# Performance work log

Hardware: AMD Instinct MI355X
Metric: run time of the kernel (lower is better)

The kernel has to match this reference:

```python
import jax, jax.numpy as jnp
import numpy as np

GROUPS = 32
EPS = 1e-5


def group_norm(x, scale, bias):
    # x: [B, C, T]
    b, c, t = x.shape
    xg = x.reshape(b, GROUPS, c // GROUPS, t)
    mean = xg.mean(axis=(2, 3), keepdims=True)
    var = xg.var(axis=(2, 3), keepdims=True)
    xg = (xg - mean) * jax.lax.rsqrt(var + EPS)
    return xg.reshape(b, c, t) * scale[None, :, None] + bias[None, :, None]


def setup_inputs() -> dict:
    key = jax.random.key(0)
    ks = jax.random.split(key, 7)
    B, C, H, W = 8, 512, 32, 32
    x = jax.random.normal(ks[0], (B, C, H, W), dtype=jnp.float32)
    gn_scale = jnp.ones((C,), jnp.float32)
    gn_bias = jnp.zeros((C,), jnp.float32)
    qkv_w = jax.random.normal(ks[1], (3 * C, C), jnp.float32) / np.sqrt(C)
    qkv_b = jnp.zeros((3 * C,), jnp.float32)
    # proj_out is zero-initialized in the original; use small random weights
    # so the attention path contributes to the output (trained-model behavior).
    proj_w = jax.random.normal(ks[2], (C, C), jnp.float32) / np.sqrt(C)
    proj_b = jnp.zeros((C,), jnp.float32)
    return {"x": x, "gn_scale": gn_scale, "gn_bias": gn_bias,
            "qkv_w": qkv_w, "qkv_b": qkv_b, "proj_w": proj_w, "proj_b": proj_b}


def reference(x, gn_scale, gn_bias, qkv_w, qkv_b, proj_w, proj_b):
    NUM_HEADS = 8
    b, c, *spatial = x.shape
    t = int(np.prod(spatial))
    xf = x.reshape(b, c, t)                                   # [B,C,T]
    xn = group_norm(xf, gn_scale, gn_bias)
    qkv = jnp.einsum('oc,bct->bot', qkv_w, xn) + qkv_b[None, :, None]  # [B,3C,T]
    # legacy layout: reshape to heads BEFORE splitting into q,k,v thirds
    qkv = qkv.reshape(b * NUM_HEADS, -1, t)                   # [B*H, 3C/H, T]
    ch = qkv.shape[1] // 3
    q, k, v = jnp.split(qkv, 3, axis=1)                       # each [B*H, ch, T]
    scale = 1.0 / np.sqrt(np.sqrt(ch))
    w = jnp.einsum('bct,bcs->bts', q * scale, k * scale)      # [B*H, T, T]
    w = jax.nn.softmax(w.astype(jnp.float32), axis=-1).astype(w.dtype)
    h = jnp.einsum('bts,bcs->bct', w, v)                      # [B*H, ch, T]
    h = h.reshape(b, c, t)
    h = jnp.einsum('oc,bct->bot', proj_w, h) + proj_b[None, :, None]
    return (xf + h).reshape(b, c, *spatial)
```

## Files before the change

kernel.cpp:

```cpp
#include <hip/hip_runtime.h>

typedef __bf16 bf16;
typedef __attribute__((ext_vector_type(8))) __bf16 bf16x8;
typedef __attribute__((ext_vector_type(4))) __bf16 bf16x4;
typedef __attribute__((ext_vector_type(4))) float f32x4;

#define MFMA(a, b, c) __builtin_amdgcn_mfma_f32_16x16x32_bf16(a, b, c, 0, 0, 0)
#define GLOAD_LDS(g, l)                                                        \
  __builtin_amdgcn_global_load_lds(                                            \
      (const __attribute__((address_space(1))) void*)(g),                      \
      (__attribute__((address_space(3))) void*)(l), 16, 0, 0)

#if __has_builtin(__builtin_amdgcn_exp2f)
#define EXP2(x) __builtin_amdgcn_exp2f(x)
#else
#define EXP2(x) exp2f(x)
#endif

#define C1LOG 0.18033688011f

__device__ __forceinline__ int swz64(int row, int col) {
  return row * 64 + (col ^ ((row & 7) << 3));
}

__global__ __launch_bounds__(256, 2) void k_pre(
    const float* __restrict__ x, const float* __restrict__ gs,
    const float* __restrict__ gb, const float* __restrict__ qw,
    const float* __restrict__ pw, bf16* __restrict__ xnT,
    bf16* __restrict__ wq, bf16* __restrict__ wp) {
  int tid = threadIdx.x;
  if (blockIdx.x >= 256) {
    int i = (blockIdx.x - 256) * 256 + tid;
    int idx = i * 4;
    float4 v;
    bf16* o;
    if (idx < 786432) {
      v = *(const float4*)(qw + idx);
      o = wq + idx;
    } else {
      int j = idx - 786432;
      v = *(const float4*)(pw + j);
      o = wp + j;
    }
    o[0] = (bf16)v.x; o[1] = (bf16)v.y; o[2] = (bf16)v.z; o[3] = (bf16)v.w;
    return;
  }
  __shared__ float xs[16 * 1024];
  __shared__ float red[2][4];
  int blk = blockIdx.x;
  int b = blk >> 5, g = blk & 31;
  const float* xp = x + ((size_t)(b * 512 + g * 16)) * 1024;
  float s = 0.f, ss = 0.f;
  for (int i = tid; i < 4096; i += 256) {
    float4 v = ((const float4*)xp)[i];
    *(float4*)&xs[i * 4] = v;
    s += v.x + v.y + v.z + v.w;
    ss += v.x * v.x + v.y * v.y + v.z * v.z + v.w * v.w;
  }
#pragma unroll
  for (int m = 1; m < 64; m <<= 1) {
    s += __shfl_xor(s, m);
    ss += __shfl_xor(ss, m);
  }
  int wid = tid >> 6;
  if ((tid & 63) == 0) { red[0][wid] = s; red[1][wid] = ss; }
  __syncthreads();
  float fs = red[0][0] + red[0][1] + red[0][2] + red[0][3];
  float fss = red[1][0] + red[1][1] + red[1][2] + red[1][3];
  float mean = fs * (1.f / 16384.f);
  float var = fss * (1.f / 16384.f) - mean * mean;
  float inv = rsqrtf(var + 1e-5f);
  float a_[16], b_[16];
#pragma unroll
  for (int cl = 0; cl < 16; ++cl) {
    float sc = gs[g * 16 + cl] * inv;
    a_[cl] = sc;
    b_[cl] = gb[g * 16 + cl] - mean * sc;
  }
  int t0 = tid * 4;
  bf16 tmp[4][16];
#pragma unroll
  for (int cl = 0; cl < 16; ++cl) {
    float4 v = *(float4*)&xs[cl * 1024 + t0];
    tmp[0][cl] = (bf16)(v.x * a_[cl] + b_[cl]);
    tmp[1][cl] = (bf16)(v.y * a_[cl] + b_[cl]);
    tmp[2][cl] = (bf16)(v.z * a_[cl] + b_[cl]);
    tmp[3][cl] = (bf16)(v.w * a_[cl] + b_[cl]);
  }
  bf16* outp = xnT + (size_t)b * 1024 * 512 + g * 16;
#pragma unroll
  for (int k = 0; k < 4; ++k) {
    *(bf16x8*)(outp + (size_t)(t0 + k) * 512) = *(bf16x8*)&tmp[k][0];
    *(bf16x8*)(outp + (size_t)(t0 + k) * 512 + 8) = *(bf16x8*)&tmp[k][8];
  }
}

__global__ void k_qkv(const bf16* __restrict__ xnT, const bf16* __restrict__ wq,
                      const float* __restrict__ qb, bf16* __restrict__ qkvT,
                      bf16* __restrict__ vTout) {
  int bid = blockIdx.x;
  int swz = (bid & 7) * 96 + (bid >> 3);
  int nt = swz % 12, mt = swz / 12;
  int tid = threadIdx.x, lane = tid & 63;
  int wid = tid >> 6, wr = wid >> 1, wc = wid & 1;
  int lr = lane & 15, lk8 = (lane >> 4) * 8, prow4 = (lane >> 4) * 4;
  __shared__ __align__(16) bf16 lA[8192], lB[8192];
  const bf16* Ab = xnT + (size_t)mt * 128 * 512;
  const bf16* Bb = wq + (size_t)nt * 128 * 512;
  f32x4 acc[4][4] = {};
  int ubase = tid & 192;
  for (int kt = 0; kt < 8; ++kt) {
    __syncthreads();
#pragma unroll
    for (int i = 0; i < 4; ++i) {
      int s = i * 256 + tid;
      int r = s >> 3, cc = (s & 7) ^ (r & 7);
      GLOAD_LDS(Ab + (size_t)r * 512 + kt * 64 + cc * 8, lA + (i * 256 + ubase) * 8);
      GLOAD_LDS(Bb + (size_t)r * 512 + kt * 64 + cc * 8, lB + (i * 256 + ubase) * 8);
    }
    __syncthreads();
#pragma unroll
    for (int ksl = 0; ksl < 2; ++ksl) {
      bf16x8 aF[4], bF[4];
#pragma unroll
      for (int m = 0; m < 4; ++m)
        aF[m] = *(bf16x8*)&lA[swz64(wr * 64 + m * 16 + lr, ksl * 32 + lk8)];
#pragma unroll
      for (int n = 0; n < 4; ++n)
        bF[n] = *(bf16x8*)&lB[swz64(wc * 64 + n * 16 + lr, ksl * 32 + lk8)];
      __builtin_amdgcn_s_setprio(1);
#pragma unroll
      for (int m = 0; m < 4; ++m)
#pragma unroll
        for (int n = 0; n < 4; ++n) acc[m][n] = MFMA(aF[m], bF[n], acc[m][n]);
      __builtin_amdgcn_s_setprio(0);
    }
  }
#pragma unroll
  for (int n = 0; n < 4; ++n) {
    int o = nt * 128 + wc * 64 + n * 16 + lr;
    float bias = qb[o];
    int hh = o / 192;
    int om = o - hh * 192;
    bool isv = om >= 128;
    float scl = (om >= 64 && om < 128) ? C1LOG : 1.0f;
    int c = om - 128;
#pragma unroll
    for (int m = 0; m < 4; ++m) {
      int row0 = mt * 128 + wr * 64 + m * 16 + prow4;
      if (isv) {
        int bb = row0 >> 10, t0 = row0 & 1023;
        bf16x4 v4;
#pragma unroll
        for (int r = 0; r < 4; ++r) v4[r] = (bf16)(acc[m][n][r] + bias);
        *(bf16x4*)&vTout[(((size_t)bb * 8 + hh) * 64 + c) * 1024 + t0] = v4;
      } else {
#pragma unroll
        for (int r = 0; r < 4; ++r)
          qkvT[(size_t)(row0 + r) * 1536 + o] = (bf16)((acc[m][n][r] + bias) * scl);
      }
    }
  }
}

__global__ __launch_bounds__(512, 4) void k_attn(const bf16* __restrict__ qkvT,
                                                 const bf16* __restrict__ vT,
                                                 bf16* __restrict__ hT) {
  int d = blockIdx.x;
  int head = (d & 7) * 8 + (d >> 6);
  int qt = (d >> 3) & 7;
  int b = head >> 3, hh = head & 7;
  int tid = threadIdx.x, lane = tid & 63, wid = tid >> 6;
  int lr = lane & 15, hi = lane >> 4, lk8 = hi * 8;

  __shared__ __align__(16) bf16 KT[2][8192];
  __shared__ __align__(16) bf16 VTl[2][8192];
  __shared__ __align__(16) bf16 PT[8][1024];

  const bf16* qbase = qkvT + (size_t)b * 1024 * 1536 + hh * 192;
  const bf16* kbase = qbase + 64;
  const bf16* vbase = vT + (size_t)head * 64 * 1024;

  int tq = qt * 128 + wid * 16 + lr;
  bf16x8 qf0 = *(const bf16x8*)(qbase + (size_t)tq * 1536 + lk8);
  bf16x8 qf1 = *(const bf16x8*)(qbase + (size_t)tq * 1536 + 32 + lk8);

  f32x4 hacc[4] = {};
  f32x4 lsum = {};
  float m2 = -1e30f;

  int rr8 = tid >> 3;
  int cc_ = (tid & 7) ^ (rr8 & 7);
  const bf16* ksrcT = kbase + (size_t)rr8 * 1536 + cc_ * 8;
  const bf16* vsrcT = vbase + (size_t)rr8 * 1024 + cc_ * 8;
  int ldst = wid * 512;

  bf16x8 ones;
#pragma unroll
  for (int j = 0; j < 8; ++j) ones[j] = (bf16)1.0f;

  GLOAD_LDS(ksrcT, KT[0] + ldst);
  GLOAD_LDS(ksrcT + (size_t)64 * 1536, KT[0] + 4096 + ldst);
  GLOAD_LDS(vsrcT, VTl[0] + ldst);
  GLOAD_LDS(vsrcT + 64, VTl[0] + 4096 + ldst);

  for (int it = 0; it < 8; ++it) {
    int cur = it & 1;
    asm volatile("s_waitcnt vmcnt(0)" ::: "memory");
    __builtin_amdgcn_s_barrier();
    __builtin_amdgcn_sched_barrier(0);
    if (it < 7) {
      size_t sb = (size_t)(it + 1) * 128;
      const bf16* kp = ksrcT + sb * 1536;
      const bf16* vp = vsrcT + sb;
      GLOAD_LDS(kp, KT[cur ^ 1] + ldst);
      GLOAD_LDS(kp + (size_t)64 * 1536, KT[cur ^ 1] + 4096 + ldst);
      GLOAD_LDS(vp, VTl[cur ^ 1] + ldst);
      GLOAD_LDS(vp + 64, VTl[cur ^ 1] + 4096 + ldst);
    }
    f32x4 sc[8];
#pragma unroll
    for (int n = 0; n < 8; ++n) sc[n] = f32x4{0.f, 0.f, 0.f, 0.f};
    __builtin_amdgcn_s_setprio(1);
#pragma unroll
    for (int n = 0; n < 8; ++n) {
      bf16x8 kA0 = *(bf16x8*)&KT[cur][swz64(n * 16 + lr, lk8)];
      bf16x8 kA1 = *(bf16x8*)&KT[cur][swz64(n * 16 + lr, 32 + lk8)];
      sc[n] = MFMA(kA0, qf0, sc[n]);
      sc[n] = MFMA(kA1, qf1, sc[n]);
    }
    __builtin_amdgcn_s_setprio(0);
    float a0 = fmaxf(fmaxf(sc[0][0], sc[0][1]), fmaxf(sc[0][2], sc[0][3]));
    float a1 = fmaxf(fmaxf(sc[1][0], sc[1][1]), fmaxf(sc[1][2], sc[1][3]));
    float a2 = fmaxf(fmaxf(sc[2][0], sc[2][1]), fmaxf(sc[2][2], sc[2][3]));
    float a3 = fmaxf(fmaxf(sc[3][0], sc[3][1]), fmaxf(sc[3][2], sc[3][3]));
    float a4 = fmaxf(fmaxf(sc[4][0], sc[4][1]), fmaxf(sc[4][2], sc[4][3]));
    float a5 = fmaxf(fmaxf(sc[5][0], sc[5][1]), fmaxf(sc[5][2], sc[5][3]));
    float a6 = fmaxf(fmaxf(sc[6][0], sc[6][1]), fmaxf(sc[6][2], sc[6][3]));
    float a7 = fmaxf(fmaxf(sc[7][0], sc[7][1]), fmaxf(sc[7][2], sc[7][3]));
    float tm = fmaxf(fmaxf(fmaxf(a0, a1), fmaxf(a2, a3)),
                     fmaxf(fmaxf(a4, a5), fmaxf(a6, a7)));
    tm = fmaxf(tm, __shfl_xor(tm, 16));
    tm = fmaxf(tm, __shfl_xor(tm, 32));
    if (__any(tm > m2 + 7.213f)) {
      float mn = fmaxf(m2, tm);
      float al = EXP2(m2 - mn);
      m2 = mn;
      lsum[0] *= al; lsum[1] *= al; lsum[2] *= al; lsum[3] *= al;
#pragma unroll
      for (int n = 0; n < 4; ++n) {
        hacc[n][0] *= al; hacc[n][1] *= al; hacc[n][2] *= al; hacc[n][3] *= al;
      }
    }
#pragma unroll
    for (int h = 0; h < 2; ++h) {
#pragma unroll
      for (int n4 = 0; n4 < 4; ++n4) {
        int n = 4 * h + n4;
        bf16x4 p4;
        p4[0] = (bf16)EXP2(sc[n][0] - m2);
        p4[1] = (bf16)EXP2(sc[n][1] - m2);
        p4[2] = (bf16)EXP2(sc[n][2] - m2);
        p4[3] = (bf16)EXP2(sc[n][3] - m2);
        *(bf16x4*)&PT[wid][swz64(lr, n4 * 16 + hi * 4)] = p4;
      }
      asm volatile("s_waitcnt lgkmcnt(0)" ::: "memory");
      __builtin_amdgcn_sched_barrier(0);
      bf16x8 pa0 = *(bf16x8*)&PT[wid][swz64(lr, lk8)];
      bf16x8 pa1 = *(bf16x8*)&PT[wid][swz64(lr, 32 + lk8)];
      const bf16* vb = VTl[cur] + h * 4096;
      __builtin_amdgcn_s_setprio(1);
#pragma unroll
      for (int n4 = 0; n4 < 4; ++n4) {
        bf16x8 vA0 = *(bf16x8*)&vb[swz64(n4 * 16 + lr, lk8)];
        bf16x8 vA1 = *(bf16x8*)&vb[swz64(n4 * 16 + lr, 32 + lk8)];
        hacc[n4] = MFMA(vA0, pa0, hacc[n4]);
        hacc[n4] = MFMA(vA1, pa1, hacc[n4]);
      }
      lsum = MFMA(ones, pa0, lsum);
      lsum = MFMA(ones, pa1, lsum);
      __builtin_amdgcn_s_setprio(0);
    }
  }
  float invl = 1.f / lsum[0];
  bf16* dst = hT + ((size_t)b * 1024 + tq) * 512 + hh * 64 + hi * 4;
#pragma unroll
  for (int n = 0; n < 4; ++n) {
    bf16x4 o4;
#pragma unroll
    for (int r = 0; r < 4; ++r) o4[r] = (bf16)(hacc[n][r] * invl);
    *(bf16x4*)(dst + n * 16) = o4;
  }
}

__global__ void k_proj(const bf16* __restrict__ hT, const bf16* __restrict__ wp,
                       const float* __restrict__ pb, const float* __restrict__ x,
                       float* __restrict__ out) {
  int bid = blockIdx.x;
  int swz = (bid & 7) * 64 + (bid >> 3);
  int nt = swz & 7, mt = swz >> 3;
  int tid = threadIdx.x, lane = tid & 63;
  int wid = tid >> 6, wr = wid >> 1, wc = wid & 1;
  int lr = lane & 15, lk8 = (lane >> 4) * 8, prow4 = (lane >> 4) * 4;
  __shared__ __align__(16) bf16 lA[8192], lB[4096];
  const bf16* Ab = hT + (size_t)mt * 128 * 512;
  const bf16* Bb = wp + (size_t)nt * 64 * 512;
  f32x4 acc[4][2] = {};
  int ubase = tid & 192;
  for (int kt = 0; kt < 8; ++kt) {
    __syncthreads();
#pragma unroll
    for (int i = 0; i < 4; ++i) {
      int s = i * 256 + tid;
      int r = s >> 3, cc = (s & 7) ^ (r & 7);
      GLOAD_LDS(Ab + (size_t)r * 512 + kt * 64 + cc * 8, lA + (i * 256 + ubase) * 8);
    }
#pragma unroll
    for (int i = 0; i < 2; ++i) {
      int s = i * 256 + tid;
      int r = s >> 3, cc = (s & 7) ^ (r & 7);
      GLOAD_LDS(Bb + (size_t)r * 512 + kt * 64 + cc * 8, lB + (i * 256 + ubase) * 8);
    }
    __syncthreads();
#pragma unroll
    for (int ksl = 0; ksl < 2; ++ksl) {
      bf16x8 aF[4], bF[2];
#pragma unroll
      for (int m = 0; m < 4; ++m)
        aF[m] = *(bf16x8*)&lA[swz64(wr * 64 + m * 16 + lr, ksl * 32 + lk8)];
#pragma unroll
      for (int n = 0; n < 2; ++n)
        bF[n] = *(bf16x8*)&lB[swz64(wc * 32 + n * 16 + lr, ksl * 32 + lk8)];
      __builtin_amdgcn_s_setprio(1);
#pragma unroll
      for (int m = 0; m < 4; ++m)
#pragma unroll
        for (int n = 0; n < 2; ++n) acc[m][n] = MFMA(aF[m], bF[n], acc[m][n]);
      __builtin_amdgcn_s_setprio(0);
    }
  }
#pragma unroll
  for (int n = 0; n < 2; ++n) {
    int o = nt * 64 + wc * 32 + n * 16 + lr;
    float bias = pb[o];
#pragma unroll
    for (int m = 0; m < 4; ++m) {
      int row0 = mt * 128 + wr * 64 + m * 16 + prow4;
      int bb = row0 >> 10, t0 = row0 & 1023;
      size_t off = ((size_t)bb * 512 + o) * 1024 + t0;
      float4 xv = *(const float4*)(x + off);
      float4 rr;
      rr.x = acc[m][n][0] + xv.x + bias;
      rr.y = acc[m][n][1] + xv.y + bias;
      rr.z = acc[m][n][2] + xv.z + bias;
      rr.w = acc[m][n][3] + xv.w + bias;
      *(float4*)(out + off) = rr;
    }
  }
}

extern "C" void kernel_launch(void* const* d_in, const int* in_sizes, int n_in,
                              void* d_out, int out_size, void* d_ws, size_t ws_size,
                              hipStream_t stream) {
  const float* x = (const float*)d_in[0];
  const float* gs = (const float*)d_in[1];
  const float* gb = (const float*)d_in[2];
  const float* qw = (const float*)d_in[3];
  const float* qb = (const float*)d_in[4];
  const float* pw = (const float*)d_in[5];
  const float* pb = (const float*)d_in[6];
  float* out = (float*)d_out;
  char* ws = (char*)d_ws;
  bf16* xnT  = (bf16*)(ws);
  bf16* qkvT = (bf16*)(ws + 8388608);
  bf16* vT   = (bf16*)(ws + 33554432);
  bf16* hT   = (bf16*)(ws + 41943040);
  bf16* wq   = (bf16*)(ws + 50331648);
  bf16* wp   = (bf16*)(ws + 51904512);

  k_pre<<<1280, 256, 0, stream>>>(x, gs, gb, qw, pw, xnT, wq, wp);
  k_qkv<<<768, 256, 0, stream>>>(xnT, wq, qb, qkvT, vT);
  k_attn<<<512, 512, 0, stream>>>(qkvT, vT, hT);
  k_proj<<<512, 256, 0, stream>>>(hT, wp, pb, x, out);
}
```

Measured before the change: 74.09 us.

## Process two query sub-tiles per wave in attention to reuse K/V fragments

The attention kernel now runs 4 waves of 256 threads per block instead of 8 waves. Each wave handles 32 query rows as two 16-row groups, so every K and V fragment read from LDS feeds twice as many MFMAs. The global-to-LDS loads are split across more iterations per thread to match the smaller block. This raises register pressure, from two sets of score and accumulator tiles, and halves the number of waves per block available to hide latency.

```diff
diff --git a/kernel.cpp b/kernel.cpp
--- a/kernel.cpp
+++ b/kernel.cpp
@@ -163,7 +163,7 @@
   }
 }
 
-__global__ __launch_bounds__(512, 4) void k_attn(const bf16* __restrict__ qkvT,
+__global__ __launch_bounds__(256, 2) void k_attn(const bf16* __restrict__ qkvT,
                                                  const bf16* __restrict__ vT,
                                                  bf16* __restrict__ hT) {
   int d = blockIdx.x;
@@ -181,28 +181,37 @@
   const bf16* kbase = qbase + 64;
   const bf16* vbase = vT + (size_t)head * 64 * 1024;
 
-  int tq = qt * 128 + wid * 16 + lr;
-  bf16x8 qf0 = *(const bf16x8*)(qbase + (size_t)tq * 1536 + lk8);
-  bf16x8 qf1 = *(const bf16x8*)(qbase + (size_t)tq * 1536 + 32 + lk8);
-
-  f32x4 hacc[4] = {};
-  f32x4 lsum = {};
-  float m2 = -1e30f;
+  int tq0 = qt * 128 + wid * 32 + lr;
+  int tq1 = tq0 + 16;
+  bf16x8 qf[2][2];
+  qf[0][0] = *(const bf16x8*)(qbase + (size_t)tq0 * 1536 + lk8);
+  qf[0][1] = *(const bf16x8*)(qbase + (size_t)tq0 * 1536 + 32 + lk8);
+  qf[1][0] = *(const bf16x8*)(qbase + (size_t)tq1 * 1536 + lk8);
+  qf[1][1] = *(const bf16x8*)(qbase + (size_t)tq1 * 1536 + 32 + lk8);
+
+  f32x4 hacc[2][4] = {};
+  f32x4 lsum[2] = {};
+  float m2[2] = {-1e30f, -1e30f};
 
   int rr8 = tid >> 3;
   int cc_ = (tid & 7) ^ (rr8 & 7);
-  const bf16* ksrcT = kbase + (size_t)rr8 * 1536 + cc_ * 8;
-  const bf16* vsrcT = vbase + (size_t)rr8 * 1024 + cc_ * 8;
+  const bf16* ks = kbase + (size_t)rr8 * 1536 + cc_ * 8;
+  const bf16* vs0 = vbase + (size_t)rr8 * 1024 + cc_ * 8;
+  const bf16* vs1 = vs0 + 64;
   int ldst = wid * 512;
 
   bf16x8 ones;
 #pragma unroll
   for (int j = 0; j < 8; ++j) ones[j] = (bf16)1.0f;
 
-  GLOAD_LDS(ksrcT, KT[0] + ldst);
-  GLOAD_LDS(ksrcT + (size_t)64 * 1536, KT[0] + 4096 + ldst);
-  GLOAD_LDS(vsrcT, VTl[0] + ldst);
-  GLOAD_LDS(vsrcT + 64, VTl[0] + 4096 + ldst);
+#pragma unroll
+  for (int i = 0; i < 4; ++i)
+    GLOAD_LDS(ks + (size_t)i * 32 * 1536, KT[0] + i * 2048 + ldst);
+#pragma unroll
+  for (int i = 0; i < 2; ++i) {
+    GLOAD_LDS(vs0 + (size_t)i * 32 * 1024, VTl[0] + i * 2048 + ldst);
+    GLOAD_LDS(vs1 + (size_t)i * 32 * 1024, VTl[0] + 4096 + i * 2048 + ldst);
+  }
 
   for (int it = 0; it < 8; ++it) {
     int cur = it & 1;
@@ -211,45 +220,60 @@
     __builtin_amdgcn_sched_barrier(0);
     if (it < 7) {
       size_t sb = (size_t)(it + 1) * 128;
-      const bf16* kp = ksrcT + sb * 1536;
-      const bf16* vp = vsrcT + sb;
-      GLOAD_LDS(kp, KT[cur ^ 1] + ldst);
-      GLOAD_LDS(kp + (size_t)64 * 1536, KT[cur ^ 1] + 4096 + ldst);
-      GLOAD_LDS(vp, VTl[cur ^ 1] + ldst);
-      GLOAD_LDS(vp + 64, VTl[cur ^ 1] + 4096 + ldst);
-    }
-    f32x4 sc[8];
-#pragma unroll
-    for (int n = 0; n < 8; ++n) sc[n] = f32x4{0.f, 0.f, 0.f, 0.f};
+      const bf16* kp = ks + sb * 1536;
+#pragma unroll
+      for (int i = 0; i < 4; ++i)
+        GLOAD_LDS(kp + (size_t)i * 32 * 1536, KT[cur ^ 1] + i * 2048 + ldst);
+#pragma unroll
+      for (int i = 0; i < 2; ++i) {
+        GLOAD_LDS(vs0 + sb + (size_t)i * 32 * 1024,
+                  VTl[cur ^ 1] + i * 2048 + ldst);
+        GLOAD_LDS(vs1 + sb + (size_t)i * 32 * 1024,
+                  VTl[cur ^ 1] + 4096 + i * 2048 + ldst);
+      }
+    }
+    f32x4 s0[8], s1[8];
+#pragma unroll
+    for (int n = 0; n < 8; ++n) {
+      s0[n] = f32x4{0.f, 0.f, 0.f, 0.f};
+      s1[n] = f32x4{0.f, 0.f, 0.f, 0.f};
+    }
     __builtin_amdgcn_s_setprio(1);
 #pragma unroll
     for (int n = 0; n < 8; ++n) {
       bf16x8 kA0 = *(bf16x8*)&KT[cur][swz64(n * 16 + lr, lk8)];
       bf16x8 kA1 = *(bf16x8*)&KT[cur][swz64(n * 16 + lr, 32 + lk8)];
-      sc[n] = MFMA(kA0, qf0, sc[n]);
-      sc[n] = MFMA(kA1, qf1, sc[n]);
+      s0[n] = MFMA(kA0, qf[0][0], s0[n]);
+      s0[n] = MFMA(kA1, qf[0][1], s0[n]);
+      s1[n] = MFMA(kA0, qf[1][0], s1[n]);
+      s1[n] = MFMA(kA1, qf[1][1], s1[n]);
     }
     __builtin_amdgcn_s_setprio(0);
-    float a0 = fmaxf(fmaxf(sc[0][0], sc[0][1]), fmaxf(sc[0][2], sc[0][3]));
-    float a1 = fmaxf(fmaxf(sc[1][0], sc[1][1]), fmaxf(sc[1][2], sc[1][3]));
-    float a2 = fmaxf(fmaxf(sc[2][0], sc[2][1]), fmaxf(sc[2][2], sc[2][3]));
-    float a3 = fmaxf(fmaxf(sc[3][0], sc[3][1]), fmaxf(sc[3][2], sc[3][3]));
-    float a4 = fmaxf(fmaxf(sc[4][0], sc[4][1]), fmaxf(sc[4][2], sc[4][3]));
-    float a5 = fmaxf(fmaxf(sc[5][0], sc[5][1]), fmaxf(sc[5][2], sc[5][3]));
-    float a6 = fmaxf(fmaxf(sc[6][0], sc[6][1]), fmaxf(sc[6][2], sc[6][3]));
-    float a7 = fmaxf(fmaxf(sc[7][0], sc[7][1]), fmaxf(sc[7][2], sc[7][3]));
-    float tm = fmaxf(fmaxf(fmaxf(a0, a1), fmaxf(a2, a3)),
-                     fmaxf(fmaxf(a4, a5), fmaxf(a6, a7)));
-    tm = fmaxf(tm, __shfl_xor(tm, 16));
-    tm = fmaxf(tm, __shfl_xor(tm, 32));
-    if (__any(tm > m2 + 7.213f)) {
-      float mn = fmaxf(m2, tm);
-      float al = EXP2(m2 - mn);
-      m2 = mn;
-      lsum[0] *= al; lsum[1] *= al; lsum[2] *= al; lsum[3] *= al;
-#pragma unroll
-      for (int n = 0; n < 4; ++n) {
-        hacc[n][0] *= al; hacc[n][1] *= al; hacc[n][2] *= al; hacc[n][3] *= al;
+#pragma unroll
+    for (int g = 0; g < 2; ++g) {
+      f32x4* sg = g ? s1 : s0;
+      float a0 = fmaxf(fmaxf(sg[0][0], sg[0][1]), fmaxf(sg[0][2], sg[0][3]));
+      float a1 = fmaxf(fmaxf(sg[1][0], sg[1][1]), fmaxf(sg[1][2], sg[1][3]));
+      float a2 = fmaxf(fmaxf(sg[2][0], sg[2][1]), fmaxf(sg[2][2], sg[2][3]));
+      float a3 = fmaxf(fmaxf(sg[3][0], sg[3][1]), fmaxf(sg[3][2], sg[3][3]));
+      float a4 = fmaxf(fmaxf(sg[4][0], sg[4][1]), fmaxf(sg[4][2], sg[4][3]));
+      float a5 = fmaxf(fmaxf(sg[5][0], sg[5][1]), fmaxf(sg[5][2], sg[5][3]));
+      float a6 = fmaxf(fmaxf(sg[6][0], sg[6][1]), fmaxf(sg[6][2], sg[6][3]));
+      float a7 = fmaxf(fmaxf(sg[7][0], sg[7][1]), fmaxf(sg[7][2], sg[7][3]));
+      float tm = fmaxf(fmaxf(fmaxf(a0, a1), fmaxf(a2, a3)),
+                       fmaxf(fmaxf(a4, a5), fmaxf(a6, a7)));
+      tm = fmaxf(tm, __shfl_xor(tm, 16));
+      tm = fmaxf(tm, __shfl_xor(tm, 32));
+      if (__any(tm > m2[g] + 7.213f)) {
+        float mn = fmaxf(m2[g], tm);
+        float al = EXP2(m2[g] - mn);
+        m2[g] = mn;
+        lsum[g][0] *= al; lsum[g][1] *= al; lsum[g][2] *= al; lsum[g][3] *= al;
+#pragma unroll
+        for (int n = 0; n < 4; ++n) {
+          hacc[g][n][0] *= al; hacc[g][n][1] *= al;
+          hacc[g][n][2] *= al; hacc[g][n][3] *= al;
+        }
       }
     }
 #pragma unroll
@@ -258,38 +282,54 @@
       for (int n4 = 0; n4 < 4; ++n4) {
         int n = 4 * h + n4;
         bf16x4 p4;
-        p4[0] = (bf16)EXP2(sc[n][0] - m2);
-        p4[1] = (bf16)EXP2(sc[n][1] - m2);
-        p4[2] = (bf16)EXP2(sc[n][2] - m2);
-        p4[3] = (bf16)EXP2(sc[n][3] - m2);
-        *(bf16x4*)&PT[wid][swz64(lr, n4 * 16 + hi * 4)] = p4;
+        p4[0] = (bf16)EXP2(s0[n][0] - m2[0]);
+        p4[1] = (bf16)EXP2(s0[n][1] - m2[0]);
+        p4[2] = (bf16)EXP2(s0[n][2] - m2[0]);
+        p4[3] = (bf16)EXP2(s0[n][3] - m2[0]);
+        *(bf16x4*)&PT[wid * 2][swz64(lr, n4 * 16 + hi * 4)] = p4;
+        bf16x4 q4;
+        q4[0] = (bf16)EXP2(s1[n][0] - m2[1]);
+        q4[1] = (bf16)EXP2(s1[n][1] - m2[1]);
+        q4[2] = (bf16)EXP2(s1[n][2] - m2[1]);
+        q4[3] = (bf16)EXP2(s1[n][3] - m2[1]);
+        *(bf16x4*)&PT[wid * 2 + 1][swz64(lr, n4 * 16 + hi * 4)] = q4;
       }
       asm volatile("s_waitcnt lgkmcnt(0)" ::: "memory");
       __builtin_amdgcn_sched_barrier(0);
-      bf16x8 pa0 = *(bf16x8*)&PT[wid][swz64(lr, lk8)];
-      bf16x8 pa1 = *(bf16x8*)&PT[wid][swz64(lr, 32 + lk8)];
+      bf16x8 pa00 = *(bf16x8*)&PT[wid * 2][swz64(lr, lk8)];
+      bf16x8 pa01 = *(bf16x8*)&PT[wid * 2][swz64(lr, 32 + lk8)];
+      bf16x8 pa10 = *(bf16x8*)&PT[wid * 2 + 1][swz64(lr, lk8)];
+      bf16x8 pa11 = *(bf16x8*)&PT[wid * 2 + 1][swz64(lr, 32 + lk8)];
       const bf16* vb = VTl[cur] + h * 4096;
       __builtin_amdgcn_s_setprio(1);
 #pragma unroll
       for (int n4 = 0; n4 < 4; ++n4) {
         bf16x8 vA0 = *(bf16x8*)&vb[swz64(n4 * 16 + lr, lk8)];
         bf16x8 vA1 = *(bf16x8*)&vb[swz64(n4 * 16 + lr, 32 + lk8)];
-        hacc[n4] = MFMA(vA0, pa0, hacc[n4]);
-        hacc[n4] = MFMA(vA1, pa1, hacc[n4]);
+        hacc[0][n4] = MFMA(vA0, pa00, hacc[0][n4]);
+        hacc[0][n4] = MFMA(vA1, pa01, hacc[0][n4]);
+        hacc[1][n4] = MFMA(vA0, pa10, hacc[1][n4]);
+        hacc[1][n4] = MFMA(vA1, pa11, hacc[1][n4]);
       }
-      lsum = MFMA(ones, pa0, lsum);
-      lsum = MFMA(ones, pa1, lsum);
+      lsum[0] = MFMA(ones, pa00, lsum[0]);
+      lsum[0] = MFMA(ones, pa01, lsum[0]);
+      lsum[1] = MFMA(ones, pa10, lsum[1]);
+      lsum[1] = MFMA(ones, pa11, lsum[1]);
       __builtin_amdgcn_s_setprio(0);
     }
   }
-  float invl = 1.f / lsum[0];
-  bf16* dst = hT + ((size_t)b * 1024 + tq) * 512 + hh * 64 + hi * 4;
-#pragma unroll
-  for (int n = 0; n < 4; ++n) {
-    bf16x4 o4;
-#pragma unroll
-    for (int r = 0; r < 4; ++r) o4[r] = (bf16)(hacc[n][r] * invl);
-    *(bf16x4*)(dst + n * 16) = o4;
+#pragma unroll
+  for (int g = 0; g < 2; ++g) {
+    float invl = 1.f / lsum[g][0];
+    int tq = g ? tq1 : tq0;
+    bf16* dst = hT + ((size_t)b * 1024 + tq) * 512 + hh * 64 + hi * 4;
+#pragma unroll
+    for (int n = 0; n < 4; ++n) {
+      bf16x4 o4;
+#pragma unroll
+      for (int r = 0; r < 4; ++r) o4[r] = (bf16)(hacc[g][n][r] * invl);
+      *(bf16x4*)(dst + n * 16) = o4;
+    }
   }
 }
 
@@ -380,6 +420,6 @@
 
   k_pre<<<1280, 256, 0, stream>>>(x, gs, gb, qw, pw, xnT, wq, wp);
   k_qkv<<<768, 256, 0, stream>>>(xnT, wq, qb, qkvT, vT);
-  k_attn<<<512, 512, 0, stream>>>(qkvT, vT, hT);
+  k_attn<<<512, 256, 0, stream>>>(qkvT, vT, hT);
   k_proj<<<512, 256, 0, stream>>>(hT, wp, pb, x, out);
 }
```

Measured after the change: 75.76 us. 2.3% more time.

## Retile QKV GEMM to 256-row blocks and shrink attention blocks to 64 queries

Applied to the files above, without the earlier changes.

The QKV GEMM now uses 512-thread blocks covering 256 rows by 128 columns, which halves the grid and reuses each weight tile across twice as many rows. The attention kernel switches to 256-thread blocks handling 64 queries each, streaming K/V in 64-key chunks over 16 iterations. This doubles the attention grid to 1024 blocks and halves its LDS footprint, aiming for more resident blocks and better load balance across CUs. The cost is more barrier and loop overhead per key processed in attention, and a larger LDS tile in the GEMM.

```diff
diff --git a/kernel.cpp b/kernel.cpp
--- a/kernel.cpp
+++ b/kernel.cpp
@@ -99,24 +99,30 @@
                       const float* __restrict__ qb, bf16* __restrict__ qkvT,
                       bf16* __restrict__ vTout) {
   int bid = blockIdx.x;
-  int swz = (bid & 7) * 96 + (bid >> 3);
+  int swz = (bid & 7) * 48 + (bid >> 3);
   int nt = swz % 12, mt = swz / 12;
   int tid = threadIdx.x, lane = tid & 63;
   int wid = tid >> 6, wr = wid >> 1, wc = wid & 1;
   int lr = lane & 15, lk8 = (lane >> 4) * 8, prow4 = (lane >> 4) * 4;
-  __shared__ __align__(16) bf16 lA[8192], lB[8192];
-  const bf16* Ab = xnT + (size_t)mt * 128 * 512;
+  __shared__ __align__(16) bf16 lA[16384], lB[8192];
+  const bf16* Ab = xnT + (size_t)mt * 256 * 512;
   const bf16* Bb = wq + (size_t)nt * 128 * 512;
   f32x4 acc[4][4] = {};
-  int ubase = tid & 192;
+  int ubase = tid & 448;
+  int r8 = tid >> 3, c8 = tid & 7;
   for (int kt = 0; kt < 8; ++kt) {
     __syncthreads();
 #pragma unroll
     for (int i = 0; i < 4; ++i) {
-      int s = i * 256 + tid;
-      int r = s >> 3, cc = (s & 7) ^ (r & 7);
-      GLOAD_LDS(Ab + (size_t)r * 512 + kt * 64 + cc * 8, lA + (i * 256 + ubase) * 8);
-      GLOAD_LDS(Bb + (size_t)r * 512 + kt * 64 + cc * 8, lB + (i * 256 + ubase) * 8);
+      int r = i * 64 + r8, cc = c8 ^ (r8 & 7);
+      GLOAD_LDS(Ab + (size_t)r * 512 + kt * 64 + cc * 8,
+                lA + (i * 512 + ubase) * 8);
+    }
+#pragma unroll
+    for (int i = 0; i < 2; ++i) {
+      int r = i * 64 + r8, cc = c8 ^ (r8 & 7);
+      GLOAD_LDS(Bb + (size_t)r * 512 + kt * 64 + cc * 8,
+                lB + (i * 512 + ubase) * 8);
     }
     __syncthreads();
 #pragma unroll
@@ -147,7 +153,7 @@
     int c = om - 128;
 #pragma unroll
     for (int m = 0; m < 4; ++m) {
-      int row0 = mt * 128 + wr * 64 + m * 16 + prow4;
+      int row0 = mt * 256 + wr * 64 + m * 16 + prow4;
       if (isv) {
         int bb = row0 >> 10, t0 = row0 & 1023;
         bf16x4 v4;
@@ -163,25 +169,26 @@
   }
 }
 
-__global__ __launch_bounds__(512, 4) void k_attn(const bf16* __restrict__ qkvT,
+__global__ __launch_bounds__(256, 4) void k_attn(const bf16* __restrict__ qkvT,
                                                  const bf16* __restrict__ vT,
                                                  bf16* __restrict__ hT) {
   int d = blockIdx.x;
-  int head = (d & 7) * 8 + (d >> 6);
-  int qt = (d >> 3) & 7;
+  int within = d >> 3;
+  int head = (d & 7) * 8 + (within >> 4);
+  int qt = within & 15;
   int b = head >> 3, hh = head & 7;
   int tid = threadIdx.x, lane = tid & 63, wid = tid >> 6;
   int lr = lane & 15, hi = lane >> 4, lk8 = hi * 8;
 
-  __shared__ __align__(16) bf16 KT[2][8192];
-  __shared__ __align__(16) bf16 VTl[2][8192];
-  __shared__ __align__(16) bf16 PT[8][1024];
+  __shared__ __align__(16) bf16 KT[2][4096];
+  __shared__ __align__(16) bf16 VTl[2][4096];
+  __shared__ __align__(16) bf16 PT[4][1024];
 
   const bf16* qbase = qkvT + (size_t)b * 1024 * 1536 + hh * 192;
   const bf16* kbase = qbase + 64;
   const bf16* vbase = vT + (size_t)head * 64 * 1024;
 
-  int tq = qt * 128 + wid * 16 + lr;
+  int tq = qt * 64 + wid * 16 + lr;
   bf16x8 qf0 = *(const bf16x8*)(qbase + (size_t)tq * 1536 + lk8);
   bf16x8 qf1 = *(const bf16x8*)(qbase + (size_t)tq * 1536 + 32 + lk8);
 
@@ -191,39 +198,40 @@
 
   int rr8 = tid >> 3;
   int cc_ = (tid & 7) ^ (rr8 & 7);
-  const bf16* ksrcT = kbase + (size_t)rr8 * 1536 + cc_ * 8;
-  const bf16* vsrcT = vbase + (size_t)rr8 * 1024 + cc_ * 8;
+  const bf16* ks = kbase + (size_t)rr8 * 1536 + cc_ * 8;
+  const bf16* vs = vbase + (size_t)rr8 * 1024 + cc_ * 8;
   int ldst = wid * 512;
 
   bf16x8 ones;
 #pragma unroll
   for (int j = 0; j < 8; ++j) ones[j] = (bf16)1.0f;
 
-  GLOAD_LDS(ksrcT, KT[0] + ldst);
-  GLOAD_LDS(ksrcT + (size_t)64 * 1536, KT[0] + 4096 + ldst);
-  GLOAD_LDS(vsrcT, VTl[0] + ldst);
-  GLOAD_LDS(vsrcT + 64, VTl[0] + 4096 + ldst);
-
-  for (int it = 0; it < 8; ++it) {
+#pragma unroll
+  for (int i = 0; i < 2; ++i) {
+    GLOAD_LDS(ks + (size_t)i * 32 * 1536, KT[0] + i * 2048 + ldst);
+    GLOAD_LDS(vs + (size_t)i * 32 * 1024, VTl[0] + i * 2048 + ldst);
+  }
+
+  for (int it = 0; it < 16; ++it) {
     int cur = it & 1;
     asm volatile("s_waitcnt vmcnt(0)" ::: "memory");
     __builtin_amdgcn_s_barrier();
     __builtin_amdgcn_sched_barrier(0);
-    if (it < 7) {
-      size_t sb = (size_t)(it + 1) * 128;
-      const bf16* kp = ksrcT + sb * 1536;
-      const bf16* vp = vsrcT + sb;
-      GLOAD_LDS(kp, KT[cur ^ 1] + ldst);
-      GLOAD_LDS(kp + (size_t)64 * 1536, KT[cur ^ 1] + 4096 + ldst);
-      GLOAD_LDS(vp, VTl[cur ^ 1] + ldst);
-      GLOAD_LDS(vp + 64, VTl[cur ^ 1] + 4096 + ldst);
-    }
-    f32x4 sc[8];
-#pragma unroll
-    for (int n = 0; n < 8; ++n) sc[n] = f32x4{0.f, 0.f, 0.f, 0.f};
+    if (it < 15) {
+      size_t sb = (size_t)(it + 1) * 64;
+#pragma unroll
+      for (int i = 0; i < 2; ++i) {
+        GLOAD_LDS(ks + (sb + i * 32) * 1536, KT[cur ^ 1] + i * 2048 + ldst);
+        GLOAD_LDS(vs + sb + (size_t)i * 32 * 1024,
+                  VTl[cur ^ 1] + i * 2048 + ldst);
+      }
+    }
+    f32x4 sc[4];
+#pragma unroll
+    for (int n = 0; n < 4; ++n) sc[n] = f32x4{0.f, 0.f, 0.f, 0.f};
     __builtin_amdgcn_s_setprio(1);
 #pragma unroll
-    for (int n = 0; n < 8; ++n) {
+    for (int n = 0; n < 4; ++n) {
       bf16x8 kA0 = *(bf16x8*)&KT[cur][swz64(n * 16 + lr, lk8)];
       bf16x8 kA1 = *(bf16x8*)&KT[cur][swz64(n * 16 + lr, 32 + lk8)];
       sc[n] = MFMA(kA0, qf0, sc[n]);
@@ -234,12 +242,7 @@
     float a1 = fmaxf(fmaxf(sc[1][0], sc[1][1]), fmaxf(sc[1][2], sc[1][3]));
     float a2 = fmaxf(fmaxf(sc[2][0], sc[2][1]), fmaxf(sc[2][2], sc[2][3]));
     float a3 = fmaxf(fmaxf(sc[3][0], sc[3][1]), fmaxf(sc[3][2], sc[3][3]));
-    float a4 = fmaxf(fmaxf(sc[4][0], sc[4][1]), fmaxf(sc[4][2], sc[4][3]));
-    float a5 = fmaxf(fmaxf(sc[5][0], sc[5][1]), fmaxf(sc[5][2], sc[5][3]));
-    float a6 = fmaxf(fmaxf(sc[6][0], sc[6][1]), fmaxf(sc[6][2], sc[6][3]));
-    float a7 = fmaxf(fmaxf(sc[7][0], sc[7][1]), fmaxf(sc[7][2], sc[7][3]));
-    float tm = fmaxf(fmaxf(fmaxf(a0, a1), fmaxf(a2, a3)),
-                     fmaxf(fmaxf(a4, a5), fmaxf(a6, a7)));
+    float tm = fmaxf(fmaxf(a0, a1), fmaxf(a2, a3));
     tm = fmaxf(tm, __shfl_xor(tm, 16));
     tm = fmaxf(tm, __shfl_xor(tm, 32));
     if (__any(tm > m2 + 7.213f)) {
@@ -253,34 +256,29 @@
       }
     }
 #pragma unroll
-    for (int h = 0; h < 2; ++h) {
-#pragma unroll
-      for (int n4 = 0; n4 < 4; ++n4) {
-        int n = 4 * h + n4;
-        bf16x4 p4;
-        p4[0] = (bf16)EXP2(sc[n][0] - m2);
-        p4[1] = (bf16)EXP2(sc[n][1] - m2);
-        p4[2] = (bf16)EXP2(sc[n][2] - m2);
-        p4[3] = (bf16)EXP2(sc[n][3] - m2);
-        *(bf16x4*)&PT[wid][swz64(lr, n4 * 16 + hi * 4)] = p4;
-      }
-      asm volatile("s_waitcnt lgkmcnt(0)" ::: "memory");
-      __builtin_amdgcn_sched_barrier(0);
-      bf16x8 pa0 = *(bf16x8*)&PT[wid][swz64(lr, lk8)];
-      bf16x8 pa1 = *(bf16x8*)&PT[wid][swz64(lr, 32 + lk8)];
-      const bf16* vb = VTl[cur] + h * 4096;
-      __builtin_amdgcn_s_setprio(1);
-#pragma unroll
-      for (int n4 = 0; n4 < 4; ++n4) {
-        bf16x8 vA0 = *(bf16x8*)&vb[swz64(n4 * 16 + lr, lk8)];
-        bf16x8 vA1 = *(bf16x8*)&vb[swz64(n4 * 16 + lr, 32 + lk8)];
-        hacc[n4] = MFMA(vA0, pa0, hacc[n4]);
-        hacc[n4] = MFMA(vA1, pa1, hacc[n4]);
-      }
-      lsum = MFMA(ones, pa0, lsum);
-      lsum = MFMA(ones, pa1, lsum);
-      __builtin_amdgcn_s_setprio(0);
-    }
+    for (int n = 0; n < 4; ++n) {
+      bf16x4 p4;
+      p4[0] = (bf16)EXP2(sc[n][0] - m2);
+      p4[1] = (bf16)EXP2(sc[n][1] - m2);
+      p4[2] = (bf16)EXP2(sc[n][2] - m2);
+      p4[3] = (bf16)EXP2(sc[n][3] - m2);
+      *(bf16x4*)&PT[wid][swz64(lr, n * 16 + hi * 4)] = p4;
+    }
+    asm volatile("s_waitcnt lgkmcnt(0)" ::: "memory");
+    __builtin_amdgcn_sched_barrier(0);
+    bf16x8 pa0 = *(bf16x8*)&PT[wid][swz64(lr, lk8)];
+    bf16x8 pa1 = *(bf16x8*)&PT[wid][swz64(lr, 32 + lk8)];
+    __builtin_amdgcn_s_setprio(1);
+#pragma unroll
+    for (int n = 0; n < 4; ++n) {
+      bf16x8 vA0 = *(bf16x8*)&VTl[cur][swz64(n * 16 + lr, lk8)];
+      bf16x8 vA1 = *(bf16x8*)&VTl[cur][swz64(n * 16 + lr, 32 + lk8)];
+      hacc[n] = MFMA(vA0, pa0, hacc[n]);
+      hacc[n] = MFMA(vA1, pa1, hacc[n]);
+    }
+    lsum = MFMA(ones, pa0, lsum);
+    lsum = MFMA(ones, pa1, lsum);
+    __builtin_amdgcn_s_setprio(0);
   }
   float invl = 1.f / lsum[0];
   bf16* dst = hT + ((size_t)b * 1024 + tq) * 512 + hh * 64 + hi * 4;
@@ -379,7 +377,7 @@
   bf16* wp   = (bf16*)(ws + 51904512);
 
   k_pre<<<1280, 256, 0, stream>>>(x, gs, gb, qw, pw, xnT, wq, wp);
-  k_qkv<<<768, 256, 0, stream>>>(xnT, wq, qb, qkvT, vT);
-  k_attn<<<512, 512, 0, stream>>>(qkvT, vT, hT);
+  k_qkv<<<384, 512, 0, stream>>>(xnT, wq, qb, qkvT, vT);
+  k_attn<<<1024, 256, 0, stream>>>(qkvT, vT, hT);
   k_proj<<<512, 256, 0, stream>>>(hT, wp, pb, x, out);
 }
```

Result: slower. 79.55 us (+7.4%).

## Read attention K from global directly; double-buffer projection GEMM tiles

Applied to the files above, without the earlier changes.

In the attention kernel, the K tile is no longer staged through a double-buffered LDS array. Each wave now loads its K fragments straight from global memory into registers inside the score loop, which frees 32KB of LDS per block and removes the K async copies. In the projection kernel, A and B tiles are double-buffered in LDS: the next K-slice is prefetched while the current one is being multiplied, so there is one barrier per iteration instead of two. The risk is that the direct K loads are not prefetched, so their global/L2 latency is exposed, and all 8 waves fetch the same K data redundantly.

```diff
diff --git a/kernel.cpp b/kernel.cpp
--- a/kernel.cpp
+++ b/kernel.cpp
@@ -173,7 +173,6 @@
   int tid = threadIdx.x, lane = tid & 63, wid = tid >> 6;
   int lr = lane & 15, hi = lane >> 4, lk8 = hi * 8;
 
-  __shared__ __align__(16) bf16 KT[2][8192];
   __shared__ __align__(16) bf16 VTl[2][8192];
   __shared__ __align__(16) bf16 PT[8][1024];
 
@@ -191,16 +190,15 @@
 
   int rr8 = tid >> 3;
   int cc_ = (tid & 7) ^ (rr8 & 7);
-  const bf16* ksrcT = kbase + (size_t)rr8 * 1536 + cc_ * 8;
   const bf16* vsrcT = vbase + (size_t)rr8 * 1024 + cc_ * 8;
   int ldst = wid * 512;
 
+  const bf16* kln = kbase + (size_t)lr * 1536 + hi * 8;
+
   bf16x8 ones;
 #pragma unroll
   for (int j = 0; j < 8; ++j) ones[j] = (bf16)1.0f;
 
-  GLOAD_LDS(ksrcT, KT[0] + ldst);
-  GLOAD_LDS(ksrcT + (size_t)64 * 1536, KT[0] + 4096 + ldst);
   GLOAD_LDS(vsrcT, VTl[0] + ldst);
   GLOAD_LDS(vsrcT + 64, VTl[0] + 4096 + ldst);
 
@@ -211,21 +209,18 @@
     __builtin_amdgcn_sched_barrier(0);
     if (it < 7) {
       size_t sb = (size_t)(it + 1) * 128;
-      const bf16* kp = ksrcT + sb * 1536;
-      const bf16* vp = vsrcT + sb;
-      GLOAD_LDS(kp, KT[cur ^ 1] + ldst);
-      GLOAD_LDS(kp + (size_t)64 * 1536, KT[cur ^ 1] + 4096 + ldst);
-      GLOAD_LDS(vp, VTl[cur ^ 1] + ldst);
-      GLOAD_LDS(vp + 64, VTl[cur ^ 1] + 4096 + ldst);
-    }
+      GLOAD_LDS(vsrcT + sb, VTl[cur ^ 1] + ldst);
+      GLOAD_LDS(vsrcT + sb + 64, VTl[cur ^ 1] + 4096 + ldst);
+    }
+    const bf16* kp = kln + (size_t)it * 128 * 1536;
     f32x4 sc[8];
 #pragma unroll
     for (int n = 0; n < 8; ++n) sc[n] = f32x4{0.f, 0.f, 0.f, 0.f};
     __builtin_amdgcn_s_setprio(1);
 #pragma unroll
     for (int n = 0; n < 8; ++n) {
-      bf16x8 kA0 = *(bf16x8*)&KT[cur][swz64(n * 16 + lr, lk8)];
-      bf16x8 kA1 = *(bf16x8*)&KT[cur][swz64(n * 16 + lr, 32 + lk8)];
+      bf16x8 kA0 = *(const bf16x8*)(kp + (size_t)n * 16 * 1536);
+      bf16x8 kA1 = *(const bf16x8*)(kp + (size_t)n * 16 * 1536 + 32);
       sc[n] = MFMA(kA0, qf0, sc[n]);
       sc[n] = MFMA(kA1, qf1, sc[n]);
     }
@@ -302,35 +297,50 @@
   int tid = threadIdx.x, lane = tid & 63;
   int wid = tid >> 6, wr = wid >> 1, wc = wid & 1;
   int lr = lane & 15, lk8 = (lane >> 4) * 8, prow4 = (lane >> 4) * 4;
-  __shared__ __align__(16) bf16 lA[8192], lB[4096];
+  __shared__ __align__(16) bf16 lA[2][8192], lB[2][4096];
   const bf16* Ab = hT + (size_t)mt * 128 * 512;
   const bf16* Bb = wp + (size_t)nt * 64 * 512;
   f32x4 acc[4][2] = {};
   int ubase = tid & 192;
+  int rr8 = tid >> 3;
+  int cc8 = (tid & 7) ^ (rr8 & 7);
+#pragma unroll
+  for (int i = 0; i < 4; ++i) {
+    int r = i * 32 + rr8;
+    GLOAD_LDS(Ab + (size_t)r * 512 + cc8 * 8, lA[0] + (i * 256 + ubase) * 8);
+  }
+#pragma unroll
+  for (int i = 0; i < 2; ++i) {
+    int r = i * 32 + rr8;
+    GLOAD_LDS(Bb + (size_t)r * 512 + cc8 * 8, lB[0] + (i * 256 + ubase) * 8);
+  }
+  __syncthreads();
   for (int kt = 0; kt < 8; ++kt) {
-    __syncthreads();
-#pragma unroll
-    for (int i = 0; i < 4; ++i) {
-      int s = i * 256 + tid;
-      int r = s >> 3, cc = (s & 7) ^ (r & 7);
-      GLOAD_LDS(Ab + (size_t)r * 512 + kt * 64 + cc * 8, lA + (i * 256 + ubase) * 8);
-    }
-#pragma unroll
-    for (int i = 0; i < 2; ++i) {
-      int s = i * 256 + tid;
-      int r = s >> 3, cc = (s & 7) ^ (r & 7);
-      GLOAD_LDS(Bb + (size_t)r * 512 + kt * 64 + cc * 8, lB + (i * 256 + ubase) * 8);
-    }
-    __syncthreads();
+    int cur = kt & 1;
+    if (kt < 7) {
+      int ktn = kt + 1;
+#pragma unroll
+      for (int i = 0; i < 4; ++i) {
+        int r = i * 32 + rr8;
+        GLOAD_LDS(Ab + (size_t)r * 512 + ktn * 64 + cc8 * 8,
+                  lA[cur ^ 1] + (i * 256 + ubase) * 8);
+      }
+#pragma unroll
+      for (int i = 0; i < 2; ++i) {
+        int r = i * 32 + rr8;
+        GLOAD_LDS(Bb + (size_t)r * 512 + ktn * 64 + cc8 * 8,
+                  lB[cur ^ 1] + (i * 256 + ubase) * 8);
+      }
+    }
 #pragma unroll
     for (int ksl = 0; ksl < 2; ++ksl) {
       bf16x8 aF[4], bF[2];
 #pragma unroll
       for (int m = 0; m < 4; ++m)
-        aF[m] = *(bf16x8*)&lA[swz64(wr * 64 + m * 16 + lr, ksl * 32 + lk8)];
+        aF[m] = *(bf16x8*)&lA[cur][swz64(wr * 64 + m * 16 + lr, ksl * 32 + lk8)];
 #pragma unroll
       for (int n = 0; n < 2; ++n)
-        bF[n] = *(bf16x8*)&lB[swz64(wc * 32 + n * 16 + lr, ksl * 32 + lk8)];
+        bF[n] = *(bf16x8*)&lB[cur][swz64(wc * 32 + n * 16 + lr, ksl * 32 + lk8)];
       __builtin_amdgcn_s_setprio(1);
 #pragma unroll
       for (int m = 0; m < 4; ++m)
@@ -338,6 +348,7 @@
         for (int n = 0; n < 2; ++n) acc[m][n] = MFMA(aF[m], bF[n], acc[m][n]);
       __builtin_amdgcn_s_setprio(0);
     }
+    __syncthreads();
   }
 #pragma unroll
   for (int n = 0; n < 2; ++n) {
```

After: 114.1 us. 1.54x slower.
